# Kernel tuning notes

Measured on AMD Instinct MI355X. Metric: run time of the kernel, lower is better.

## Reference

```python
import jax, jax.numpy as jnp
import numpy as np

BIG = 1e8  # replaces inf entries in the cost matrix, as in the torch module


def _hungarian(cost):
    """Min-cost bipartite assignment for an (n, m) cost matrix with n <= m.
    Returns, for each row i, the assigned column (same optimum as
    scipy.optimize.linear_sum_assignment; rows come back in sorted order).
    Classic O(n*m^2) shortest-augmenting-path algorithm with potentials."""
    n, m = cost.shape
    INF = np.inf
    u = np.zeros(n + 1)
    v = np.zeros(m + 1)
    p = np.zeros(m + 1, dtype=np.int64)   # p[j]: row matched to col j (1-based; 0 = free)
    way = np.zeros(m + 1, dtype=np.int64)
    for i in range(1, n + 1):
        p[0] = i
        j0 = 0
        minv = np.full(m + 1, INF)
        used = np.zeros(m + 1, dtype=bool)
        while True:
            used[j0] = True
            i0 = p[j0]
            cur = cost[i0 - 1, :] - u[i0] - v[1:]
            free = ~used[1:]
            better = free & (cur < minv[1:])
            minv[1:] = np.where(better, cur, minv[1:])
            way[1:] = np.where(better, j0, way[1:])
            cand = np.where(free, minv[1:], INF)
            j1 = int(np.argmin(cand)) + 1
            delta = cand[j1 - 1]
            u[p[used]] += delta
            v[used] -= delta
            minv[~used] -= delta
            j0 = j1
            if p[j0] == 0:
                break
        while j0 != 0:
            j1 = int(way[j0])
            p[j0] = p[j1]
            j0 = j1
    ans = np.zeros(n, dtype=np.int64)
    for j in range(1, m + 1):
        if p[j] != 0:
            ans[p[j] - 1] = j - 1
    return ans


def _matched_labels(outputs, gold, weight):
    """Per-sample Hungarian matching on the restricted-softmax NLL cost,
    exactly as the torch module: cost[b] = -log_softmax(outputs[b][:, gold[b]], 1) * w[gold[b]].
    Matching is detached (host-side), mirroring scipy linear_sum_assignment."""
    B, S, C = outputs.shape
    idx = jnp.broadcast_to(gold[:, None, :], (B, S, S))
    sub = jnp.take_along_axis(outputs, idx, axis=2)                  # [B,S,S] logits at gold cols
    cost = -jax.nn.log_softmax(sub, axis=2) * weight[gold][:, None, :]
    cost = jnp.where(jnp.isinf(cost), BIG, cost)
    cost_np = np.asarray(cost, dtype=np.float64)
    gold_np = np.asarray(gold)
    match = np.empty_like(gold_np)
    for b in range(B):
        col = _hungarian(cost_np[b])                                 # row i -> gold column
        match[b] = gold_np[b][col]
    return jnp.asarray(match)


def setup_inputs() -> dict:
    key = jax.random.key(0)
    k1, k2 = jax.random.split(key)
    B, S, C = 128, 20, 32000
    outputs = jax.random.normal(k1, (B, S, C), dtype=jnp.float32)
    gold_label_ids = jax.random.randint(k2, (B, S), 0, C)
    mask = jnp.ones((B, S), dtype=bool)
    weight = jnp.ones((C,), dtype=jnp.float32)
    return {"outputs": outputs, "gold_label_ids": gold_label_ids, "mask": mask, "weight": weight}


def reference(outputs, gold_label_ids, mask, weight):
    eps = 1e-8
    match = _matched_labels(outputs, gold_label_ids, weight)         # [B,S] matched class ids
    logp = jax.nn.log_softmax(outputs, axis=-1)                      # [B,S,C]
    nll = -jnp.take_along_axis(logp, match[..., None], axis=2)[..., 0] * weight[match]
    m = mask.reshape(-1).astype(outputs.dtype)
    loss = nll.reshape(-1) * m
    return jnp.sum(loss) / (jnp.sum(m) + eps)
```

## Files before the change

### kernel.cpp

```cpp
#include <hip/hip_runtime.h>
#include <hip/hip_bf16.h>
#include <math.h>

#define NB 128
#define NS 20
#define NC 32000
#define NROWS (NB * NS)
#define NBLOCKS 1280

static __device__ __forceinline__ float fmin_x1(float x) {
    int t = __builtin_amdgcn_update_dpp(0, __float_as_int(x), 0xB1, 0xf, 0xf, true);
    return fminf(x, __int_as_float(t));
}
static __device__ __forceinline__ float fmin_x2(float x) {
    int t = __builtin_amdgcn_update_dpp(0, __float_as_int(x), 0x4E, 0xf, 0xf, true);
    return fminf(x, __int_as_float(t));
}
static __device__ __forceinline__ float fmin_x4(float x) {
    int t = __builtin_amdgcn_ds_swizzle(__float_as_int(x), 0x101F);
    return fminf(x, __int_as_float(t));
}
static __device__ __forceinline__ float fmin_x8(float x) {
    int t = __builtin_amdgcn_ds_swizzle(__float_as_int(x), 0x201F);
    return fminf(x, __int_as_float(t));
}
static __device__ __forceinline__ float fmin_x16(float x) {
    int t = __builtin_amdgcn_ds_swizzle(__float_as_int(x), 0x401F);
    return fminf(x, __int_as_float(t));
}
static __device__ __forceinline__ float readlane_f(float x, int lane) {
    return __int_as_float(__builtin_amdgcn_readlane(__float_as_int(x), lane));
}

__global__ __launch_bounds__(256) void mega_kernel(
        const float* __restrict__ outputs,
        const int* __restrict__ gold,
        const float* __restrict__ weight,
        int* __restrict__ match_col,
        float* __restrict__ sub_ws,
        float* __restrict__ logZ) {

    __shared__ float smx[4], ssm[4];
    const int bid = blockIdx.x;

    if (bid < NB) {
        const int b = bid;
        const int* g = gold + b * NS;
        __shared__ float cst[NS * NS];
        __shared__ float lzs[NS];

        for (int e = threadIdx.x; e < NS * NS; e += 256) {
            int i = e / NS, j = e - i * NS;
            float x = outputs[(size_t)(b * NS + i) * NC + g[j]];
            cst[e] = x;
            sub_ws[(size_t)(b * NS + i) * NS + j] = x;
        }
        __syncthreads();
        if (threadIdx.x < NS) {
            int i = threadIdx.x;
            float mx = cst[i * NS];
#pragma unroll
            for (int j = 1; j < NS; ++j) mx = fmaxf(mx, cst[i * NS + j]);
            float s = 0.f;
#pragma unroll
            for (int j = 0; j < NS; ++j) s += __expf(cst[i * NS + j] - mx);
            lzs[i] = mx + __logf(s);
        }
        __syncthreads();
        for (int e = threadIdx.x; e < NS * NS; e += 256) {
            int i = e / NS, j = e - i * NS;
            float c = -(cst[e] - lzs[i]) * weight[g[j]];
            if (isinf(c)) c = 1e8f;
            cst[e] = c;
        }
        __syncthreads();

        if (threadIdx.x < 64) {
            const int lane = threadIdx.x;
            const float FINF = INFINITY;
            float up_j = 0.f, v_j = 0.f;
            int p_j = 0, way_j = 0;
            const bool is_col = (lane >= 1 && lane <= NS);

            for (int i = 1; i <= NS; ++i) {
                if (lane == 0) { p_j = i; up_j = 0.f; }
                int j0 = 0;
                float minv_j = FINF;
                bool used_j = false;
                while (true) {
                    int pp = __builtin_amdgcn_readlane(p_j, j0);
                    if (pp == 0) break;
                    if (lane == j0) used_j = true;
                    float upp = readlane_f(up_j, j0);
                    float cv = cst[is_col ? (pp - 1) * NS + (lane - 1) : 0];
                    if (is_col && !used_j) {
                        float curv = cv - upp - v_j;
                        if (curv < minv_j) { minv_j = curv; way_j = j0; }
                    }
                    float cand = (is_col && !used_j) ? minv_j : FINF;
                    float mval = fmin_x16(fmin_x8(fmin_x4(fmin_x2(fmin_x1(cand)))));
                    unsigned long long bal = __ballot(cand == mval) & 0xFFFFFFFFull;
                    int j1 = __ffsll(bal) - 1;
                    float delta = mval;
                    if (used_j) { up_j += delta; v_j -= delta; }
                    else if (is_col) minv_j -= delta;
                    j0 = j1;
                }
                while (j0 != 0) {
                    int   j1   = __builtin_amdgcn_readlane(way_j, j0);
                    int   pj1  = __builtin_amdgcn_readlane(p_j, j1);
                    float upj1 = readlane_f(up_j, j1);
                    if (lane == j0) { p_j = pj1; up_j = upj1; }
                    j0 = j1;
                }
            }
            if (is_col && p_j != 0) {
                match_col[b * NS + (p_j - 1)] = lane - 1;
            }
        }
        __syncthreads();
    }

    int r0, nr;
    if (bid < 128)      { r0 = 2432 + bid;          nr = 1; }
    else if (bid < 256) { r0 = (bid - 128) * 3;     nr = 3; }
    else                { r0 = 384 + (bid - 256) * 2; nr = 2; }

    for (int rr = 0; rr < nr; ++rr) {
        const int row = r0 + rr;
        const float4* rp = (const float4*)(outputs + (size_t)row * NC);
        const int n4 = NC / 4;
        const int nfull = (n4 / 1024) * 1024;

        float m = -INFINITY;
        float s = 0.f;
        for (int base = 0; base < nfull; base += 1024) {
            int i0 = base + threadIdx.x;
            float4 a = rp[i0];
            float4 bq = rp[i0 + 256];
            float4 c = rp[i0 + 512];
            float4 d = rp[i0 + 768];
            float m4 = fmaxf(fmaxf(fmaxf(a.x, a.y), fmaxf(a.z, a.w)),
                             fmaxf(fmaxf(bq.x, bq.y), fmaxf(bq.z, bq.w)));
            m4 = fmaxf(m4, fmaxf(fmaxf(fmaxf(c.x, c.y), fmaxf(c.z, c.w)),
                                 fmaxf(fmaxf(d.x, d.y), fmaxf(d.z, d.w))));
            float nm = fmaxf(m, m4);
            float sl = __expf(a.x - nm) + __expf(a.y - nm)
                     + __expf(a.z - nm) + __expf(a.w - nm);
            sl += __expf(bq.x - nm) + __expf(bq.y - nm)
                + __expf(bq.z - nm) + __expf(bq.w - nm);
            sl += __expf(c.x - nm) + __expf(c.y - nm)
                + __expf(c.z - nm) + __expf(c.w - nm);
            sl += __expf(d.x - nm) + __expf(d.y - nm)
                + __expf(d.z - nm) + __expf(d.w - nm);
            s = s * __expf(m - nm) + sl;
            m = nm;
        }
        for (int idx = nfull + threadIdx.x; idx < n4; idx += 256) {
            float4 x = rp[idx];
            float m4 = fmaxf(fmaxf(x.x, x.y), fmaxf(x.z, x.w));
            float nm = fmaxf(m, m4);
            s = s * __expf(m - nm)
              + __expf(x.x - nm) + __expf(x.y - nm)
              + __expf(x.z - nm) + __expf(x.w - nm);
            m = nm;
        }
        for (int off = 1; off < 64; off <<= 1) {
            float om = __shfl_xor(m, off);
            float os = __shfl_xor(s, off);
            float nm = fmaxf(m, om);
            s = s * __expf(m - nm) + os * __expf(om - nm);
            m = nm;
        }
        __syncthreads();
        int wid = threadIdx.x >> 6;
        if ((threadIdx.x & 63) == 0) { smx[wid] = m; ssm[wid] = s; }
        __syncthreads();
        if (threadIdx.x == 0) {
            float M = smx[0], S = ssm[0];
            for (int w = 1; w < 4; ++w) {
                float om = smx[w], os = ssm[w];
                float nm = fmaxf(M, om);
                S = S * __expf(M - nm) + os * __expf(om - nm);
                M = nm;
            }
            logZ[row] = M + __logf(S);
        }
    }
}

__global__ __launch_bounds__(512) void final_kernel(
        const int* __restrict__ match_col,
        const float* __restrict__ sub_ws,
        const float* __restrict__ logZ,
        const float* __restrict__ weight,
        const int* __restrict__ gold,
        const unsigned char* __restrict__ mask,
        float* __restrict__ out) {
    double nsum = 0.0, msum = 0.0;
    for (int r = threadIdx.x; r < NROWS; r += 512) {
        int b = r / NS;
        int col = match_col[r];
        float x = sub_ws[(size_t)r * NS + col];
        float w = weight[gold[b * NS + col]];
        float nll = -(x - logZ[r]) * w;
        float mk = mask[r] ? 1.f : 0.f;
        nsum += (double)(nll * mk);
        msum += (double)mk;
    }
    for (int off = 1; off < 64; off <<= 1) {
        nsum += __shfl_xor(nsum, off);
        msum += __shfl_xor(msum, off);
    }
    __shared__ double sn[8], sm[8];
    int wid = threadIdx.x >> 6;
    if ((threadIdx.x & 63) == 0) { sn[wid] = nsum; sm[wid] = msum; }
    __syncthreads();
    if (threadIdx.x == 0) {
        double N = 0.0, M = 0.0;
        for (int w = 0; w < 8; ++w) { N += sn[w]; M += sm[w]; }
        out[0] = (float)(N / (M + 1e-8));
    }
}

extern "C" void kernel_launch(void* const* d_in, const int* in_sizes, int n_in,
                              void* d_out, int out_size, void* d_ws, size_t ws_size,
                              hipStream_t stream) {
    const float* outputs        = (const float*)d_in[0];
    const int*   gold           = (const int*)d_in[1];
    const unsigned char* mask   = (const unsigned char*)d_in[2];
    const float* weight         = (const float*)d_in[3];
    float* out = (float*)d_out;

    char* ws = (char*)d_ws;
    int*   match_col = (int*)ws;
    float* logZ      = (float*)(ws + (size_t)NROWS * 4);
    float* sub_ws    = (float*)(ws + (size_t)NROWS * 8);

    mega_kernel<<<NBLOCKS, 256, 0, stream>>>(outputs, gold, weight,
                                             match_col, sub_ws, logZ);
    final_kernel<<<1, 512, 0, stream>>>(match_col, sub_ws, logZ, weight, gold,
                                        mask, out);
}
```

Before: 69.08 us.

## Use single-wave blocks with one softmax row per block and split Hungarian blocks

Switches the main kernel from 256-thread blocks to 64-thread (single wavefront) blocks. Hungarian blocks now do only matching, and each remaining block computes logZ for exactly one row, using 8 float4 loads in flight per lane and a wave-only reduction with no shared-memory combine. The final reduction kernel also grows to 1024 threads. The aim is to stop the Hungarian blocks from also carrying softmax rows, to remove the cross-wave sync, and to raise memory-level parallelism per lane, at the cost of many more small blocks.

Measured after the change: 90.99 us. 1.32x slower.

```diff
diff --git a/kernel.cpp b/kernel.cpp
--- a/kernel.cpp
+++ b/kernel.cpp
@@ -6,7 +6,7 @@
 #define NS 20
 #define NC 32000
 #define NROWS (NB * NS)
-#define NBLOCKS 1280
+#define NBLOCKS (NB + NROWS)
 
 static __device__ __forceinline__ float fmin_x1(float x) {
     int t = __builtin_amdgcn_update_dpp(0, __float_as_int(x), 0xB1, 0xf, 0xf, true);
@@ -31,8 +31,11 @@
 static __device__ __forceinline__ float readlane_f(float x, int lane) {
     return __int_as_float(__builtin_amdgcn_readlane(__float_as_int(x), lane));
 }
-
-__global__ __launch_bounds__(256) void mega_kernel(
+static __device__ __forceinline__ float max4(float4 a) {
+    return fmaxf(fmaxf(a.x, a.y), fmaxf(a.z, a.w));
+}
+
+__global__ __launch_bounds__(64) void mega_kernel(
         const float* __restrict__ outputs,
         const int* __restrict__ gold,
         const float* __restrict__ weight,
@@ -40,8 +43,8 @@
         float* __restrict__ sub_ws,
         float* __restrict__ logZ) {
 
-    __shared__ float smx[4], ssm[4];
     const int bid = blockIdx.x;
+    const int lane = threadIdx.x;
 
     if (bid < NB) {
         const int b = bid;
@@ -49,15 +52,15 @@
         __shared__ float cst[NS * NS];
         __shared__ float lzs[NS];
 
-        for (int e = threadIdx.x; e < NS * NS; e += 256) {
+        for (int e = lane; e < NS * NS; e += 64) {
             int i = e / NS, j = e - i * NS;
             float x = outputs[(size_t)(b * NS + i) * NC + g[j]];
             cst[e] = x;
             sub_ws[(size_t)(b * NS + i) * NS + j] = x;
         }
         __syncthreads();
-        if (threadIdx.x < NS) {
-            int i = threadIdx.x;
+        if (lane < NS) {
+            int i = lane;
             float mx = cst[i * NS];
 #pragma unroll
             for (int j = 1; j < NS; ++j) mx = fmaxf(mx, cst[i * NS + j]);
@@ -67,7 +70,7 @@
             lzs[i] = mx + __logf(s);
         }
         __syncthreads();
-        for (int e = threadIdx.x; e < NS * NS; e += 256) {
+        for (int e = lane; e < NS * NS; e += 64) {
             int i = e / NS, j = e - i * NS;
             float c = -(cst[e] - lzs[i]) * weight[g[j]];
             if (isinf(c)) c = 1e8f;
@@ -75,94 +78,107 @@
         }
         __syncthreads();
 
-        if (threadIdx.x < 64) {
-            const int lane = threadIdx.x;
-            const float FINF = INFINITY;
-            float up_j = 0.f, v_j = 0.f;
-            int p_j = 0, way_j = 0;
-            const bool is_col = (lane >= 1 && lane <= NS);
-
-            for (int i = 1; i <= NS; ++i) {
-                if (lane == 0) { p_j = i; up_j = 0.f; }
-                int j0 = 0;
-                float minv_j = FINF;
-                bool used_j = false;
-                while (true) {
-                    int pp = __builtin_amdgcn_readlane(p_j, j0);
-                    if (pp == 0) break;
-                    if (lane == j0) used_j = true;
-                    float upp = readlane_f(up_j, j0);
-                    float cv = cst[is_col ? (pp - 1) * NS + (lane - 1) : 0];
-                    if (is_col && !used_j) {
-                        float curv = cv - upp - v_j;
-                        if (curv < minv_j) { minv_j = curv; way_j = j0; }
-                    }
-                    float cand = (is_col && !used_j) ? minv_j : FINF;
-                    float mval = fmin_x16(fmin_x8(fmin_x4(fmin_x2(fmin_x1(cand)))));
-                    unsigned long long bal = __ballot(cand == mval) & 0xFFFFFFFFull;
-                    int j1 = __ffsll(bal) - 1;
-                    float delta = mval;
-                    if (used_j) { up_j += delta; v_j -= delta; }
-                    else if (is_col) minv_j -= delta;
-                    j0 = j1;
+        const float FINF = INFINITY;
+        float up_j = 0.f, v_j = 0.f;
+        int p_j = 0, way_j = 0;
+        const bool is_col = (lane >= 1 && lane <= NS);
+
+        for (int i = 1; i <= NS; ++i) {
+            if (lane == 0) { p_j = i; up_j = 0.f; }
+            int j0 = 0;
+            float minv_j = FINF;
+            bool used_j = false;
+            while (true) {
+                int pp = __builtin_amdgcn_readlane(p_j, j0);
+                if (pp == 0) break;
+                if (lane == j0) used_j = true;
+                float upp = readlane_f(up_j, j0);
+                float cv = cst[is_col ? (pp - 1) * NS + (lane - 1) : 0];
+                if (is_col && !used_j) {
+                    float curv = cv - upp - v_j;
+                    if (curv < minv_j) { minv_j = curv; way_j = j0; }
                 }
-                while (j0 != 0) {
-                    int   j1   = __builtin_amdgcn_readlane(way_j, j0);
-                    int   pj1  = __builtin_amdgcn_readlane(p_j, j1);
-                    float upj1 = readlane_f(up_j, j1);
-                    if (lane == j0) { p_j = pj1; up_j = upj1; }
-                    j0 = j1;
-                }
+                float cand = (is_col && !used_j) ? minv_j : FINF;
+                float mval = fmin_x16(fmin_x8(fmin_x4(fmin_x2(fmin_x1(cand)))));
+                unsigned long long bal = __ballot(cand == mval) & 0xFFFFFFFFull;
+                int j1 = __ffsll(bal) - 1;
+                float delta = mval;
+                if (used_j) { up_j += delta; v_j -= delta; }
+                else if (is_col) minv_j -= delta;
+                j0 = j1;
             }
-            if (is_col && p_j != 0) {
-                match_col[b * NS + (p_j - 1)] = lane - 1;
+            while (j0 != 0) {
+                int   j1   = __builtin_amdgcn_readlane(way_j, j0);
+                int   pj1  = __builtin_amdgcn_readlane(p_j, j1);
+                float upj1 = readlane_f(up_j, j1);
+                if (lane == j0) { p_j = pj1; up_j = upj1; }
+                j0 = j1;
             }
         }
-        __syncthreads();
-    }
-
-    int r0, nr;
-    if (bid < 128)      { r0 = 2432 + bid;          nr = 1; }
-    else if (bid < 256) { r0 = (bid - 128) * 3;     nr = 3; }
-    else                { r0 = 384 + (bid - 256) * 2; nr = 2; }
-
-    for (int rr = 0; rr < nr; ++rr) {
-        const int row = r0 + rr;
+        if (is_col && p_j != 0) {
+            match_col[b * NS + (p_j - 1)] = lane - 1;
+        }
+    } else {
+        const int row = bid - NB;
         const float4* rp = (const float4*)(outputs + (size_t)row * NC);
-        const int n4 = NC / 4;
-        const int nfull = (n4 / 1024) * 1024;
 
         float m = -INFINITY;
         float s = 0.f;
-        for (int base = 0; base < nfull; base += 1024) {
-            int i0 = base + threadIdx.x;
+        for (int it = 0; it < 15; ++it) {
+            int i0 = it * 512 + lane;
             float4 a = rp[i0];
-            float4 bq = rp[i0 + 256];
-            float4 c = rp[i0 + 512];
-            float4 d = rp[i0 + 768];
-            float m4 = fmaxf(fmaxf(fmaxf(a.x, a.y), fmaxf(a.z, a.w)),
-                             fmaxf(fmaxf(bq.x, bq.y), fmaxf(bq.z, bq.w)));
-            m4 = fmaxf(m4, fmaxf(fmaxf(fmaxf(c.x, c.y), fmaxf(c.z, c.w)),
-                                 fmaxf(fmaxf(d.x, d.y), fmaxf(d.z, d.w))));
+            float4 b4 = rp[i0 + 64];
+            float4 c = rp[i0 + 128];
+            float4 d = rp[i0 + 192];
+            float4 e = rp[i0 + 256];
+            float4 f = rp[i0 + 320];
+            float4 g4 = rp[i0 + 384];
+            float4 h = rp[i0 + 448];
+            float m4 = fmaxf(fmaxf(fmaxf(max4(a), max4(b4)),
+                                   fmaxf(max4(c), max4(d))),
+                             fmaxf(fmaxf(max4(e), max4(f)),
+                                   fmaxf(max4(g4), max4(h))));
             float nm = fmaxf(m, m4);
             float sl = __expf(a.x - nm) + __expf(a.y - nm)
-                     + __expf(a.z - nm) + __expf(a.w - nm);
-            sl += __expf(bq.x - nm) + __expf(bq.y - nm)
-                + __expf(bq.z - nm) + __expf(bq.w - nm);
-            sl += __expf(c.x - nm) + __expf(c.y - nm)
-                + __expf(c.z - nm) + __expf(c.w - nm);
-            sl += __expf(d.x - nm) + __expf(d.y - nm)
-                + __expf(d.z - nm) + __expf(d.w - nm);
+                     + __expf(a.z - nm) + __expf(a.w - nm)
+                     + __expf(b4.x - nm) + __expf(b4.y - nm)
+                     + __expf(b4.z - nm) + __expf(b4.w - nm)
+                     + __expf(c.x - nm) + __expf(c.y - nm)
+                     + __expf(c.z - nm) + __expf(c.w - nm)
+                     + __expf(d.x - nm) + __expf(d.y - nm)
+                     + __expf(d.z - nm) + __expf(d.w - nm)
+                     + __expf(e.x - nm) + __expf(e.y - nm)
+                     + __expf(e.z - nm) + __expf(e.w - nm)
+                     + __expf(f.x - nm) + __expf(f.y - nm)
+                     + __expf(f.z - nm) + __expf(f.w - nm)
+                     + __expf(g4.x - nm) + __expf(g4.y - nm)
+                     + __expf(g4.z - nm) + __expf(g4.w - nm)
+                     + __expf(h.x - nm) + __expf(h.y - nm)
+                     + __expf(h.z - nm) + __expf(h.w - nm);
             s = s * __expf(m - nm) + sl;
             m = nm;
         }
-        for (int idx = nfull + threadIdx.x; idx < n4; idx += 256) {
-            float4 x = rp[idx];
-            float m4 = fmaxf(fmaxf(x.x, x.y), fmaxf(x.z, x.w));
+        {
+            int i0 = 7680 + lane;
+            float4 a = rp[i0];
+            float4 b4 = rp[i0 + 64];
+            float4 c = rp[i0 + 128];
+            float4 d = rp[i0 + 192];
+            float4 e = rp[i0 + 256];
+            float m4 = fmaxf(fmaxf(fmaxf(max4(a), max4(b4)),
+                                   fmaxf(max4(c), max4(d))), max4(e));
             float nm = fmaxf(m, m4);
-            s = s * __expf(m - nm)
-              + __expf(x.x - nm) + __expf(x.y - nm)
-              + __expf(x.z - nm) + __expf(x.w - nm);
+            float sl = __expf(a.x - nm) + __expf(a.y - nm)
+                     + __expf(a.z - nm) + __expf(a.w - nm)
+                     + __expf(b4.x - nm) + __expf(b4.y - nm)
+                     + __expf(b4.z - nm) + __expf(b4.w - nm)
+                     + __expf(c.x - nm) + __expf(c.y - nm)
+                     + __expf(c.z - nm) + __expf(c.w - nm)
+                     + __expf(d.x - nm) + __expf(d.y - nm)
+                     + __expf(d.z - nm) + __expf(d.w - nm)
+                     + __expf(e.x - nm) + __expf(e.y - nm)
+                     + __expf(e.z - nm) + __expf(e.w - nm);
+            s = s * __expf(m - nm) + sl;
             m = nm;
         }
         for (int off = 1; off < 64; off <<= 1) {
@@ -172,24 +188,11 @@
             s = s * __expf(m - nm) + os * __expf(om - nm);
             m = nm;
         }
-        __syncthreads();
-        int wid = threadIdx.x >> 6;
-        if ((threadIdx.x & 63) == 0) { smx[wid] = m; ssm[wid] = s; }
-        __syncthreads();
-        if (threadIdx.x == 0) {
-            float M = smx[0], S = ssm[0];
-            for (int w = 1; w < 4; ++w) {
-                float om = smx[w], os = ssm[w];
-                float nm = fmaxf(M, om);
-                S = S * __expf(M - nm) + os * __expf(om - nm);
-                M = nm;
-            }
-            logZ[row] = M + __logf(S);
-        }
-    }
-}
-
-__global__ __launch_bounds__(512) void final_kernel(
+        if (lane == 0) logZ[row] = m + __logf(s);
+    }
+}
+
+__global__ __launch_bounds__(1024) void final_kernel(
         const int* __restrict__ match_col,
         const float* __restrict__ sub_ws,
         const float* __restrict__ logZ,
@@ -198,7 +201,7 @@
         const unsigned char* __restrict__ mask,
         float* __restrict__ out) {
     double nsum = 0.0, msum = 0.0;
-    for (int r = threadIdx.x; r < NROWS; r += 512) {
+    for (int r = threadIdx.x; r < NROWS; r += 1024) {
         int b = r / NS;
         int col = match_col[r];
         float x = sub_ws[(size_t)r * NS + col];
@@ -212,13 +215,13 @@
         nsum += __shfl_xor(nsum, off);
         msum += __shfl_xor(msum, off);
     }
-    __shared__ double sn[8], sm[8];
+    __shared__ double sn[16], sm[16];
     int wid = threadIdx.x >> 6;
     if ((threadIdx.x & 63) == 0) { sn[wid] = nsum; sm[wid] = msum; }
     __syncthreads();
     if (threadIdx.x == 0) {
         double N = 0.0, M = 0.0;
-        for (int w = 0; w < 8; ++w) { N += sn[w]; M += sm[w]; }
+        for (int w = 0; w < 16; ++w) { N += sn[w]; M += sm[w]; }
         out[0] = (float)(N / (M + 1e-8));
     }
 }
@@ -237,8 +240,8 @@
     float* logZ      = (float*)(ws + (size_t)NROWS * 4);
     float* sub_ws    = (float*)(ws + (size_t)NROWS * 8);
 
-    mega_kernel<<<NBLOCKS, 256, 0, stream>>>(outputs, gold, weight,
-                                             match_col, sub_ws, logZ);
-    final_kernel<<<1, 512, 0, stream>>>(match_col, sub_ws, logZ, weight, gold,
-                                        mask, out);
-}
+    mega_kernel<<<NBLOCKS, 64, 0, stream>>>(outputs, gold, weight,
+                                            match_col, sub_ws, logZ);
+    final_kernel<<<1, 1024, 0, stream>>>(match_col, sub_ws, logZ, weight, gold,
+                                         mask, out);
+}
```
